# Kernel optimization log

Hardware: AMD Instinct MI355X
Metric: run time of the kernel (lower is better)

The kernel has to match this reference:

```python
import jax, jax.numpy as jnp
import numpy as np
import math

D_MODEL = 1024
N_HEADS = 16
D_KV = 64
NUM_BUCKETS = 32
MAX_DISTANCE = 128
BATCH = 4
SEQ = 2048


def _relative_position_bucket(relative_position, num_buckets=NUM_BUCKETS, max_distance=MAX_DISTANCE):
    # bidirectional=True (encoder)
    num_buckets //= 2
    relative_buckets = (relative_position > 0).astype(jnp.int32) * num_buckets
    rp = jnp.abs(relative_position)
    max_exact = num_buckets // 2
    is_small = rp < max_exact
    rp_safe = jnp.maximum(rp, 1)  # avoid log(0); masked by is_small anyway
    rp_if_large = max_exact + (
        jnp.log(rp_safe.astype(jnp.float32) / max_exact)
        / math.log(max_distance / max_exact)
        * (num_buckets - max_exact)
    ).astype(jnp.int32)
    rp_if_large = jnp.minimum(rp_if_large, num_buckets - 1)
    relative_buckets += jnp.where(is_small, rp, rp_if_large)
    return relative_buckets


def compute_bias(rel_bias, q_len, k_len):
    context = jnp.arange(q_len)[:, None]
    memory = jnp.arange(k_len)[None, :]
    buckets = _relative_position_bucket(memory - context)  # [q, k]
    values = rel_bias[buckets]                              # [q, k, h]
    return jnp.transpose(values, (2, 0, 1))[None]           # [1, h, q, k]


def setup_inputs() -> dict:
    key = jax.random.key(0)
    ks = jax.random.split(key, 6)
    s = 1.0 / math.sqrt(D_MODEL)
    return {
        "hidden_states": jax.random.normal(ks[0], (BATCH, SEQ, D_MODEL), jnp.float32),
        "wq": jax.random.normal(ks[1], (D_MODEL, N_HEADS * D_KV), jnp.float32) * s,
        "wk": jax.random.normal(ks[2], (D_MODEL, N_HEADS * D_KV), jnp.float32) * s,
        "wv": jax.random.normal(ks[3], (D_MODEL, N_HEADS * D_KV), jnp.float32) * s,
        "wo": jax.random.normal(ks[4], (N_HEADS * D_KV, D_MODEL), jnp.float32) * s,
        "rel_bias": jax.random.normal(ks[5], (NUM_BUCKETS, N_HEADS), jnp.float32) * 0.5,
    }


def reference(hidden_states, wq, wk, wv, wo, rel_bias):
    B, S, _ = hidden_states.shape

    def shape(x):  # [B,S,H*Dk] -> [B,H,S,Dk]
        return x.reshape(B, S, N_HEADS, D_KV).transpose(0, 2, 1, 3)

    q = shape(hidden_states @ wq)
    k = shape(hidden_states @ wk)
    v = shape(hidden_states @ wv)

    # NOTE: T5 does NOT scale by 1/sqrt(d_kv)
    scores = jnp.einsum("bhqd,bhkd->bhqk", q, k)
    position_bias = compute_bias(rel_bias, S, S)  # [1,H,S,S]
    scores = scores + position_bias
    attn = jax.nn.softmax(scores.astype(jnp.float32), axis=-1).astype(scores.dtype)
    ctx = jnp.einsum("bhqk,bhkd->bhqd", attn, v)
    ctx = ctx.transpose(0, 2, 1, 3).reshape(B, S, N_HEADS * D_KV)
    return ctx @ wo
```

## Files before the change

kernel.cpp:

```cpp
#include <hip/hip_runtime.h>
#include <hip/hip_bf16.h>

typedef unsigned short u16;
typedef unsigned int   u32;
typedef __bf16 bf16x8 __attribute__((ext_vector_type(8)));
typedef float  f32x4  __attribute__((ext_vector_type(4)));
typedef u16    u16x8  __attribute__((ext_vector_type(8)));
typedef u16    u16x4  __attribute__((ext_vector_type(4)));

#define MFMA16(a,b,c) __builtin_amdgcn_mfma_f32_16x16x32_bf16(a,b,c,0,0,0)
#define LOG2E 1.4426950408889634f

__device__ __forceinline__ u16 f2b(float f) {
    u32 u = __builtin_bit_cast(u32, f);
    u32 r = (u + 0x7FFFu + ((u >> 16) & 1u)) >> 16;
    return (u16)r;
}

typedef const __attribute__((address_space(1))) u32* gaddr_t;
typedef __attribute__((address_space(3))) u32*       laddr_t;
__device__ __forceinline__ void gl_lds16(const void* g, void* l) {
    __builtin_amdgcn_global_load_lds((gaddr_t)g, (laddr_t)l, 16, 0, 0);
}

__global__ __launch_bounds__(256) void prep_kernel(
        const float* __restrict__ H, const float* __restrict__ wq,
        const float* __restrict__ wk, const float* __restrict__ wv,
        const float* __restrict__ wo, const float* __restrict__ rel_bias,
        u16* __restrict__ Hb, u16* __restrict__ Wt, u16* __restrict__ Wot,
        float* __restrict__ tab) {
    __shared__ u16 tile[64 * 72];
    int bi = blockIdx.x;
    int t = threadIdx.x;
    if (bi < 4096) {
        int i = (bi * 256 + t) * 8;
        float4 a = *(const float4*)(H + i);
        float4 b = *(const float4*)(H + i + 4);
        u16x8 o = { f2b(a.x), f2b(a.y), f2b(a.z), f2b(a.w),
                    f2b(b.x), f2b(b.y), f2b(b.z), f2b(b.w) };
        *(u16x8*)(Hb + i) = o;
    } else if (bi < 5120) {
        int g2 = bi - 4096;
        int g = g2 >> 8, rem = g2 & 255;
        int n0 = (rem >> 4) * 64, k0 = (rem & 15) * 64;
        const float* src = (g == 0) ? wq : (g == 1) ? wk : (g == 2) ? wv : wo;
        u16* dst = (g < 3) ? (Wt + g * 1048576) : Wot;
#pragma unroll
        for (int rr = 0; rr < 4; ++rr) {
            int idx = rr * 256 + t;
            int kr = idx >> 4, c = idx & 15;
            float4 v = *(const float4*)(src + (k0 + kr) * 1024 + n0 + c * 4);
            u16x4 o = { f2b(v.x), f2b(v.y), f2b(v.z), f2b(v.w) };
            *(u16x4*)&tile[kr * 72 + c * 4] = o;
        }
        __syncthreads();
#pragma unroll
        for (int rr = 0; rr < 2; ++rr) {
            int idx = rr * 256 + t;
            int n = idx >> 3, c = idx & 7;
            u16x8 o;
#pragma unroll
            for (int j = 0; j < 8; ++j) o[j] = tile[(c * 8 + j) * 72 + n];
            *(u16x8*)(dst + (n0 + n) * 1024 + k0 + c * 8) = o;
        }
    } else {
        int i = (bi - 5120) * 256 + t;
        int h = i >> 12;
        int idx = i & 4095;
        int delta = idx - 2048;
        int bucket = (delta > 0) ? 16 : 0;
        int rp = delta < 0 ? -delta : delta;
        if (rp < 8) {
            bucket += rp;
        } else {
            double v = log((double)rp / 8.0) / log(16.0) * 8.0;
            int tt = (int)v;
            int b2 = 8 + tt;
            bucket += (b2 < 15) ? b2 : 15;
        }
        tab[h * 4096 + idx] = rel_bias[bucket * 16 + h] * LOG2E;
    }
}

template <int MODE>
__global__ __launch_bounds__(256) void gemm_bt(
        const u16* __restrict__ A, const u16* __restrict__ Bt, int K, int N,
        u16* __restrict__ q_out, u16* __restrict__ k_out, u16* __restrict__ v_out,
        float* __restrict__ f_out) {
    __shared__ u16 As[128 * 32];
    __shared__ u16 Bs[128 * 32];
    __shared__ u16 vt_tile[MODE == 0 ? 128 * 136 : 1];
    int t = threadIdx.x;
    int lane = t & 63, w = t >> 6;
    int wm = w & 1, wn = w >> 1;
    int ln = lane & 15, quad = lane >> 4;
    int m0 = blockIdx.x * 128, n0 = blockIdx.y * 128;
    const u16* Ab = A + m0 * K;
    const u16* Bb = Bt + n0 * K;
    f32x4 acc[4][4] = {};
    int nk = K >> 5;
    for (int kt = 0; kt < nk; ++kt) {
        int k0 = kt * 32;
#pragma unroll
        for (int rr = 0; rr < 2; ++rr) {
            int idx = rr * 256 + t;
            int row = idx >> 2, c = (idx & 3) ^ (row & 3);
            gl_lds16(Ab + row * K + k0 + c * 8, ((char*)As) + idx * 16);
            gl_lds16(Bb + row * K + k0 + c * 8, ((char*)Bs) + idx * 16);
        }
        __syncthreads();
        bf16x8 af[4], bfr[4];
#pragma unroll
        for (int mb = 0; mb < 4; ++mb) {
            int row = wm * 64 + mb * 16 + ln;
            af[mb] = *(const bf16x8*)&As[row * 32 + ((quad ^ (row & 3)) << 3)];
        }
#pragma unroll
        for (int nb = 0; nb < 4; ++nb) {
            int row = wn * 64 + nb * 16 + ln;
            bfr[nb] = *(const bf16x8*)&Bs[row * 32 + ((quad ^ (row & 3)) << 3)];
        }
#pragma unroll
        for (int mb = 0; mb < 4; ++mb)
#pragma unroll
            for (int nb = 0; nb < 4; ++nb)
                acc[mb][nb] = MFMA16(af[mb], bfr[nb], acc[mb][nb]);
        __syncthreads();
    }
    if (MODE == 0 && n0 >= 2048) {
#pragma unroll
        for (int mb = 0; mb < 4; ++mb)
#pragma unroll
            for (int nb = 0; nb < 4; ++nb)
#pragma unroll
                for (int r = 0; r < 4; ++r) {
                    int np = wn * 64 + nb * 16 + ln;
                    int mp = wm * 64 + mb * 16 + quad * 4 + r;
                    vt_tile[np * 136 + mp] = f2b(acc[mb][nb][r]);
                }
        __syncthreads();
        int h0 = (n0 >> 6) & 15;
        int b = m0 >> 11;
        int s0 = m0 & 2047;
#pragma unroll
        for (int j = 0; j < 8; ++j) {
            int e = j * 256 + t;
            int d_all = e >> 4;
            int sc = e & 15;
            int hh = h0 + (d_all >> 6);
            int d = d_all & 63;
            u16x8 val = *(const u16x8*)&vt_tile[d_all * 136 + sc * 8];
            *(u16x8*)(v_out + (b * 16 + hh) * 131072 + d * 2048 + s0 + sc * 8) = val;
        }
    } else {
#pragma unroll
        for (int mb = 0; mb < 4; ++mb)
#pragma unroll
            for (int nb = 0; nb < 4; ++nb)
#pragma unroll
                for (int r = 0; r < 4; ++r) {
                    int m = m0 + wm * 64 + mb * 16 + quad * 4 + r;
                    int n = n0 + wn * 64 + nb * 16 + ln;
                    float v = acc[mb][nb][r];
                    if (MODE == 0) {
                        int which = n >> 10, h = (n >> 6) & 15, d = n & 63;
                        int b = m >> 11, s = m & 2047;
                        u16* dst = (which == 0) ? q_out : k_out;
                        float scale = (which == 0) ? LOG2E : 1.0f;
                        dst[(((b << 4) + h) * 2048 + s) * 64 + d] = f2b(v * scale);
                    } else {
                        f_out[m * N + n] = v;
                    }
                }
    }
}

__global__ __launch_bounds__(256, 3) void attn_kernel(
        const u16* __restrict__ Qb, const u16* __restrict__ Kb,
        const u16* __restrict__ Vt, const float* __restrict__ bias_tab,
        u16* __restrict__ ctx) {
    __shared__ u16 Ks[128 * 64];
    __shared__ u16 Vs[64 * 128];
    __shared__ u16 Ps[4][16 * 64];
    __shared__ float sb[2176];
    int t = threadIdx.x;
    int lane = t & 63, w = t >> 6;
    int ln = lane & 15, quad = lane >> 4;
    int bh = blockIdx.x >> 5;
    int qtile = blockIdx.x & 31;
    int h = bh & 15, b = bh >> 4;
    int q0 = qtile * 64;

    float chi = bias_tab[h * 4096 + 2048 + 1500];
    float clo = bias_tab[h * 4096 + 2048 - 1500];

    const float* tb = bias_tab + h * 4096 + (1985 - q0);
    for (int i = t; i < 2175; i += 256) sb[i] = tb[i];

    int qa = q0 + w * 16 + ln;
    const u16* qptr = Qb + (bh * 2048 + qa) * 64 + quad * 8;
    bf16x8 qf0 = *(const bf16x8*)(qptr);
    bf16x8 qf1 = *(const bf16x8*)(qptr + 32);

    const u16* Kbase = Kb + bh * 2048 * 64;
    const u16* Vbase = Vt + bh * 64 * 2048;

    f32x4 oacc[4] = {};
    float l_i = 0.0f;
    int cb_base = 63 - w * 16 + quad * 4 - ln;
    int swl = ln & 7;

    for (int kt = 0; kt < 16; ++kt) {
        int kb0 = kt * 128;
#pragma unroll
        for (int it = 0; it < 4; ++it) {
            int idx = it * 256 + t;
            int row = idx >> 3, c = (idx & 7) ^ (row & 7);
            gl_lds16(Kbase + (kb0 + row) * 64 + c * 8, ((char*)Ks) + idx * 16);
        }
#pragma unroll
        for (int it = 0; it < 4; ++it) {
            int idx = it * 256 + t;
            int row = idx >> 4, c = (idx & 15) ^ (row & 7);
            gl_lds16(Vbase + row * 2048 + kb0 + c * 8, ((char*)Vs) + idx * 16);
        }
        __syncthreads();

        f32x4 sacc[8];
        int diff = kb0 - q0;
        if (diff >= 192 || diff <= -256) {
            float c0 = (diff > 0) ? chi : clo;
            f32x4 ci = {c0, c0, c0, c0};
#pragma unroll
            for (int nb = 0; nb < 8; ++nb) {
                int key = nb * 16 + ln;
                int sw = key & 7;
                bf16x8 kf0 = *(const bf16x8*)&Ks[key * 64 + ((quad ^ sw) << 3)];
                bf16x8 kf1 = *(const bf16x8*)&Ks[key * 64 + (((quad ^ 4) ^ sw) << 3)];
                f32x4 scc = MFMA16(kf0, qf0, ci);
                sacc[nb] = MFMA16(kf1, qf1, scc);
            }
        } else {
            int cb = kb0 + cb_base;
#pragma unroll
            for (int nb = 0; nb < 8; ++nb) {
                int key = nb * 16 + ln;
                int sw = key & 7;
                const float* bp = &sb[cb + nb * 16];
                f32x4 ci = {bp[0], bp[1], bp[2], bp[3]};
                bf16x8 kf0 = *(const bf16x8*)&Ks[key * 64 + ((quad ^ sw) << 3)];
                bf16x8 kf1 = *(const bf16x8*)&Ks[key * 64 + (((quad ^ 4) ^ sw) << 3)];
                f32x4 scc = MFMA16(kf0, qf0, ci);
                sacc[nb] = MFMA16(kf1, qf1, scc);
            }
        }

        float p[8][4];
        float ls0 = 0.f, ls1 = 0.f, ls2 = 0.f, ls3 = 0.f;
#pragma unroll
        for (int nb = 0; nb < 8; ++nb) {
            float e0 = __builtin_amdgcn_exp2f(sacc[nb][0]);
            float e1 = __builtin_amdgcn_exp2f(sacc[nb][1]);
            float e2 = __builtin_amdgcn_exp2f(sacc[nb][2]);
            float e3 = __builtin_amdgcn_exp2f(sacc[nb][3]);
            p[nb][0] = e0; p[nb][1] = e1; p[nb][2] = e2; p[nb][3] = e3;
            ls0 += e0; ls1 += e1; ls2 += e2; ls3 += e3;
        }
        l_i += (ls0 + ls1) + (ls2 + ls3);

        u16* pw = &Ps[w][0];
#pragma unroll
        for (int half = 0; half < 2; ++half) {
#pragma unroll
            for (int nbh = 0; nbh < 4; ++nbh) {
                int nb = half * 4 + nbh;
                u32 a0 = __builtin_bit_cast(u32, p[nb][0]) + 0x8000u;
                u32 a1 = __builtin_bit_cast(u32, p[nb][1]) + 0x8000u;
                u32 a2 = __builtin_bit_cast(u32, p[nb][2]) + 0x8000u;
                u32 a3 = __builtin_bit_cast(u32, p[nb][3]) + 0x8000u;
                u32 lo = __builtin_amdgcn_perm(a1, a0, 0x07060302);
                u32 hi = __builtin_amdgcn_perm(a3, a2, 0x07060302);
                int c = nbh * 2 + (quad >> 1);
                u32* dst = (u32*)&pw[ln * 64 + ((c ^ swl) << 3) + (quad & 1) * 4];
                dst[0] = lo;
                dst[1] = hi;
            }
#pragma unroll
            for (int kc = 0; kc < 2; ++kc) {
                bf16x8 pf = *(const bf16x8*)&pw[ln * 64 + (((kc * 4 + quad) ^ swl) << 3)];
#pragma unroll
                for (int nb = 0; nb < 4; ++nb) {
                    int d = nb * 16 + ln;
                    int vc = (half * 8 + kc * 4 + quad) ^ (d & 7);
                    bf16x8 vf = *(const bf16x8*)&Vs[d * 128 + (vc << 3)];
                    oacc[nb] = MFMA16(pf, vf, oacc[nb]);
                }
            }
        }
        __syncthreads();
    }

    l_i += __shfl_xor(l_i, 16);
    l_i += __shfl_xor(l_i, 32);
    float linv = 1.0f / l_i;
#pragma unroll
    for (int r = 0; r < 4; ++r) {
        float lr = __shfl(linv, quad * 4 + r);
        int q = q0 + w * 16 + quad * 4 + r;
#pragma unroll
        for (int nb = 0; nb < 4; ++nb)
            ctx[(b * 2048 + q) * 1024 + h * 64 + nb * 16 + ln] = f2b(oacc[nb][r] * lr);
    }
}

extern "C" void kernel_launch(void* const* d_in, const int* in_sizes, int n_in,
                              void* d_out, int out_size, void* d_ws, size_t ws_size,
                              hipStream_t stream) {
    const float* H   = (const float*)d_in[0];
    const float* wq  = (const float*)d_in[1];
    const float* wk  = (const float*)d_in[2];
    const float* wv  = (const float*)d_in[3];
    const float* wo  = (const float*)d_in[4];
    const float* rel = (const float*)d_in[5];
    float* out = (float*)d_out;

    char* ws = (char*)d_ws;
    u16* Hb    = (u16*)(ws);
    u16* Wt    = (u16*)(ws + 16777216);
    u16* Wot   = (u16*)(ws + 23068672);
    u16* Qb    = (u16*)(ws + 25165824);
    u16* Kb    = (u16*)(ws + 41943040);
    u16* Vt    = (u16*)(ws + 58720256);
    float* bias_tab = (float*)(ws + 75497472);
    u16* ctx = Hb;

    prep_kernel<<<5376, 256, 0, stream>>>(H, wq, wk, wv, wo, rel, Hb, Wt, Wot, bias_tab);
    gemm_bt<0><<<dim3(64, 24), 256, 0, stream>>>(Hb, Wt, 1024, 3072, Qb, Kb, Vt, nullptr);
    attn_kernel<<<2048, 256, 0, stream>>>(Qb, Kb, Vt, bias_tab, ctx);
    gemm_bt<1><<<dim3(64, 8), 256, 0, stream>>>(ctx, Wot, 1024, 1024, nullptr, nullptr, nullptr, out);
}
```

Baseline: 303.2 us.

## Process two 64-row query tiles per attention block to reuse K/V LDS loads

Each attention block now handles 128 queries (two 64-row sub-tiles A and B) instead of 64, so each K/V tile staged in shared memory is reused for twice as many queries. The grid is halved accordingly and the bias table window is shifted to cover both sub-tiles. The aim is to cut global-to-LDS traffic and barrier count per query. In exchange, register pressure roughly doubles for accumulators and Q fragments, which may reduce occupancy under launch bounds of 3 blocks per CU, and the grid of 1024 blocks gives fewer waves to balance across CUs.

```diff
diff --git a/kernel.cpp b/kernel.cpp
--- a/kernel.cpp
+++ b/kernel.cpp
@@ -186,27 +186,30 @@
     int t = threadIdx.x;
     int lane = t & 63, w = t >> 6;
     int ln = lane & 15, quad = lane >> 4;
-    int bh = blockIdx.x >> 5;
-    int qtile = blockIdx.x & 31;
+    int bh = blockIdx.x >> 4;
+    int qt = blockIdx.x & 15;
     int h = bh & 15, b = bh >> 4;
-    int q0 = qtile * 64;
+    int Q0 = qt * 128;
 
     float chi = bias_tab[h * 4096 + 2048 + 1500];
     float clo = bias_tab[h * 4096 + 2048 - 1500];
 
-    const float* tb = bias_tab + h * 4096 + (1985 - q0);
+    const float* tb = bias_tab + h * 4096 + (1921 - Q0);
     for (int i = t; i < 2175; i += 256) sb[i] = tb[i];
 
-    int qa = q0 + w * 16 + ln;
-    const u16* qptr = Qb + (bh * 2048 + qa) * 64 + quad * 8;
-    bf16x8 qf0 = *(const bf16x8*)(qptr);
-    bf16x8 qf1 = *(const bf16x8*)(qptr + 32);
+    const u16* qpA = Qb + (bh * 2048 + Q0 + w * 16 + ln) * 64 + quad * 8;
+    bf16x8 qfA0 = *(const bf16x8*)(qpA);
+    bf16x8 qfA1 = *(const bf16x8*)(qpA + 32);
+    const u16* qpB = qpA + 4096;
+    bf16x8 qfB0 = *(const bf16x8*)(qpB);
+    bf16x8 qfB1 = *(const bf16x8*)(qpB + 32);
 
     const u16* Kbase = Kb + bh * 2048 * 64;
     const u16* Vbase = Vt + bh * 64 * 2048;
 
-    f32x4 oacc[4] = {};
-    float l_i = 0.0f;
+    f32x4 oaccA[4] = {};
+    f32x4 oaccB[4] = {};
+    float lA = 0.0f, lB = 0.0f;
     int cb_base = 63 - w * 16 + quad * 4 - ln;
     int swl = ln & 7;
 
@@ -226,90 +229,179 @@
         }
         __syncthreads();
 
-        f32x4 sacc[8];
-        int diff = kb0 - q0;
-        if (diff >= 192 || diff <= -256) {
-            float c0 = (diff > 0) ? chi : clo;
-            f32x4 ci = {c0, c0, c0, c0};
+        {
+            f32x4 sacc[8];
+            int diff = kb0 - Q0;
+            if (diff >= 192 || diff <= -256) {
+                float c0 = (diff > 0) ? chi : clo;
+                f32x4 ci = {c0, c0, c0, c0};
+#pragma unroll
+                for (int nb = 0; nb < 8; ++nb) {
+                    int key = nb * 16 + ln;
+                    int sw = key & 7;
+                    bf16x8 kf0 = *(const bf16x8*)&Ks[key * 64 + ((quad ^ sw) << 3)];
+                    bf16x8 kf1 = *(const bf16x8*)&Ks[key * 64 + (((quad ^ 4) ^ sw) << 3)];
+                    f32x4 scc = MFMA16(kf0, qfA0, ci);
+                    sacc[nb] = MFMA16(kf1, qfA1, scc);
+                }
+            } else {
+                int cb = kb0 + cb_base + 64;
+#pragma unroll
+                for (int nb = 0; nb < 8; ++nb) {
+                    int key = nb * 16 + ln;
+                    int sw = key & 7;
+                    const float* bp = &sb[cb + nb * 16];
+                    f32x4 ci = {bp[0], bp[1], bp[2], bp[3]};
+                    bf16x8 kf0 = *(const bf16x8*)&Ks[key * 64 + ((quad ^ sw) << 3)];
+                    bf16x8 kf1 = *(const bf16x8*)&Ks[key * 64 + (((quad ^ 4) ^ sw) << 3)];
+                    f32x4 scc = MFMA16(kf0, qfA0, ci);
+                    sacc[nb] = MFMA16(kf1, qfA1, scc);
+                }
+            }
+            float p[8][4];
+            float ls0 = 0.f, ls1 = 0.f, ls2 = 0.f, ls3 = 0.f;
 #pragma unroll
             for (int nb = 0; nb < 8; ++nb) {
-                int key = nb * 16 + ln;
-                int sw = key & 7;
-                bf16x8 kf0 = *(const bf16x8*)&Ks[key * 64 + ((quad ^ sw) << 3)];
-                bf16x8 kf1 = *(const bf16x8*)&Ks[key * 64 + (((quad ^ 4) ^ sw) << 3)];
-                f32x4 scc = MFMA16(kf0, qf0, ci);
-                sacc[nb] = MFMA16(kf1, qf1, scc);
-            }
-        } else {
-            int cb = kb0 + cb_base;
+                float e0 = __builtin_amdgcn_exp2f(sacc[nb][0]);
+                float e1 = __builtin_amdgcn_exp2f(sacc[nb][1]);
+                float e2 = __builtin_amdgcn_exp2f(sacc[nb][2]);
+                float e3 = __builtin_amdgcn_exp2f(sacc[nb][3]);
+                p[nb][0] = e0; p[nb][1] = e1; p[nb][2] = e2; p[nb][3] = e3;
+                ls0 += e0; ls1 += e1; ls2 += e2; ls3 += e3;
+            }
+            lA += (ls0 + ls1) + (ls2 + ls3);
+            u16* pw = &Ps[w][0];
+#pragma unroll
+            for (int half = 0; half < 2; ++half) {
+#pragma unroll
+                for (int nbh = 0; nbh < 4; ++nbh) {
+                    int nb = half * 4 + nbh;
+                    u32 a0 = __builtin_bit_cast(u32, p[nb][0]) + 0x8000u;
+                    u32 a1 = __builtin_bit_cast(u32, p[nb][1]) + 0x8000u;
+                    u32 a2 = __builtin_bit_cast(u32, p[nb][2]) + 0x8000u;
+                    u32 a3 = __builtin_bit_cast(u32, p[nb][3]) + 0x8000u;
+                    u32 lo = __builtin_amdgcn_perm(a1, a0, 0x07060302);
+                    u32 hi = __builtin_amdgcn_perm(a3, a2, 0x07060302);
+                    int c = nbh * 2 + (quad >> 1);
+                    u32* dst = (u32*)&pw[ln * 64 + ((c ^ swl) << 3) + (quad & 1) * 4];
+                    dst[0] = lo;
+                    dst[1] = hi;
+                }
+#pragma unroll
+                for (int kc = 0; kc < 2; ++kc) {
+                    bf16x8 pf = *(const bf16x8*)&pw[ln * 64 + (((kc * 4 + quad) ^ swl) << 3)];
+#pragma unroll
+                    for (int nb = 0; nb < 4; ++nb) {
+                        int d = nb * 16 + ln;
+                        int vc = (half * 8 + kc * 4 + quad) ^ (d & 7);
+                        bf16x8 vf = *(const bf16x8*)&Vs[d * 128 + (vc << 3)];
+                        oaccA[nb] = MFMA16(pf, vf, oaccA[nb]);
+                    }
+                }
+            }
+        }
+
+        {
+            f32x4 sacc[8];
+            int diff = kb0 - Q0 - 64;
+            if (diff >= 192 || diff <= -256) {
+                float c0 = (diff > 0) ? chi : clo;
+                f32x4 ci = {c0, c0, c0, c0};
+#pragma unroll
+                for (int nb = 0; nb < 8; ++nb) {
+                    int key = nb * 16 + ln;
+                    int sw = key & 7;
+                    bf16x8 kf0 = *(const bf16x8*)&Ks[key * 64 + ((quad ^ sw) << 3)];
+                    bf16x8 kf1 = *(const bf16x8*)&Ks[key * 64 + (((quad ^ 4) ^ sw) << 3)];
+                    f32x4 scc = MFMA16(kf0, qfB0, ci);
+                    sacc[nb] = MFMA16(kf1, qfB1, scc);
+                }
+            } else {
+                int cb = kb0 + cb_base;
+#pragma unroll
+                for (int nb = 0; nb < 8; ++nb) {
+                    int key = nb * 16 + ln;
+                    int sw = key & 7;
+                    const float* bp = &sb[cb + nb * 16];
+                    f32x4 ci = {bp[0], bp[1], bp[2], bp[3]};
+                    bf16x8 kf0 = *(const bf16x8*)&Ks[key * 64 + ((quad ^ sw) << 3)];
+                    bf16x8 kf1 = *(const bf16x8*)&Ks[key * 64 + (((quad ^ 4) ^ sw) << 3)];
+                    f32x4 scc = MFMA16(kf0, qfB0, ci);
+                    sacc[nb] = MFMA16(kf1, qfB1, scc);
+                }
+            }
+            float p[8][4];
+            float ls0 = 0.f, ls1 = 0.f, ls2 = 0.f, ls3 = 0.f;
 #pragma unroll
             for (int nb = 0; nb < 8; ++nb) {
-                int key = nb * 16 + ln;
-                int sw = key & 7;
-                const float* bp = &sb[cb + nb * 16];
-                f32x4 ci = {bp[0], bp[1], bp[2], bp[3]};
-                bf16x8 kf0 = *(const bf16x8*)&Ks[key * 64 + ((quad ^ sw) << 3)];
-                bf16x8 kf1 = *(const bf16x8*)&Ks[key * 64 + (((quad ^ 4) ^ sw) << 3)];
-                f32x4 scc = MFMA16(kf0, qf0, ci);
-                sacc[nb] = MFMA16(kf1, qf1, scc);
-            }
-        }
-
-        float p[8][4];
-        float ls0 = 0.f, ls1 = 0.f, ls2 = 0.f, ls3 = 0.f;
-#pragma unroll
-        for (int nb = 0; nb < 8; ++nb) {
-            float e0 = __builtin_amdgcn_exp2f(sacc[nb][0]);
-            float e1 = __builtin_amdgcn_exp2f(sacc[nb][1]);
-            float e2 = __builtin_amdgcn_exp2f(sacc[nb][2]);
-            float e3 = __builtin_amdgcn_exp2f(sacc[nb][3]);
-            p[nb][0] = e0; p[nb][1] = e1; p[nb][2] = e2; p[nb][3] = e3;
-            ls0 += e0; ls1 += e1; ls2 += e2; ls3 += e3;
-        }
-        l_i += (ls0 + ls1) + (ls2 + ls3);
-
-        u16* pw = &Ps[w][0];
-#pragma unroll
-        for (int half = 0; half < 2; ++half) {
-#pragma unroll
-            for (int nbh = 0; nbh < 4; ++nbh) {
-                int nb = half * 4 + nbh;
-                u32 a0 = __builtin_bit_cast(u32, p[nb][0]) + 0x8000u;
-                u32 a1 = __builtin_bit_cast(u32, p[nb][1]) + 0x8000u;
-                u32 a2 = __builtin_bit_cast(u32, p[nb][2]) + 0x8000u;
-                u32 a3 = __builtin_bit_cast(u32, p[nb][3]) + 0x8000u;
-                u32 lo = __builtin_amdgcn_perm(a1, a0, 0x07060302);
-                u32 hi = __builtin_amdgcn_perm(a3, a2, 0x07060302);
-                int c = nbh * 2 + (quad >> 1);
-                u32* dst = (u32*)&pw[ln * 64 + ((c ^ swl) << 3) + (quad & 1) * 4];
-                dst[0] = lo;
-                dst[1] = hi;
-            }
-#pragma unroll
-            for (int kc = 0; kc < 2; ++kc) {
-                bf16x8 pf = *(const bf16x8*)&pw[ln * 64 + (((kc * 4 + quad) ^ swl) << 3)];
-#pragma unroll
-                for (int nb = 0; nb < 4; ++nb) {
-                    int d = nb * 16 + ln;
-                    int vc = (half * 8 + kc * 4 + quad) ^ (d & 7);
-                    bf16x8 vf = *(const bf16x8*)&Vs[d * 128 + (vc << 3)];
-                    oacc[nb] = MFMA16(pf, vf, oacc[nb]);
-                }
-            }
-        }
-        __syncthreads();
-    }
-
-    l_i += __shfl_xor(l_i, 16);
-    l_i += __shfl_xor(l_i, 32);
-    float linv = 1.0f / l_i;
-#pragma unroll
-    for (int r = 0; r < 4; ++r) {
-        float lr = __shfl(linv, quad * 4 + r);
-        int q = q0 + w * 16 + quad * 4 + r;
-#pragma unroll
-        for (int nb = 0; nb < 4; ++nb)
-            ctx[(b * 2048 + q) * 1024 + h * 64 + nb * 16 + ln] = f2b(oacc[nb][r] * lr);
+                float e0 = __builtin_amdgcn_exp2f(sacc[nb][0]);
+                float e1 = __builtin_amdgcn_exp2f(sacc[nb][1]);
+                float e2 = __builtin_amdgcn_exp2f(sacc[nb][2]);
+                float e3 = __builtin_amdgcn_exp2f(sacc[nb][3]);
+                p[nb][0] = e0; p[nb][1] = e1; p[nb][2] = e2; p[nb][3] = e3;
+                ls0 += e0; ls1 += e1; ls2 += e2; ls3 += e3;
+            }
+            lB += (ls0 + ls1) + (ls2 + ls3);
+            u16* pw = &Ps[w][0];
+#pragma unroll
+            for (int half = 0; half < 2; ++half) {
+#pragma unroll
+                for (int nbh = 0; nbh < 4; ++nbh) {
+                    int nb = half * 4 + nbh;
+                    u32 a0 = __builtin_bit_cast(u32, p[nb][0]) + 0x8000u;
+                    u32 a1 = __builtin_bit_cast(u32, p[nb][1]) + 0x8000u;
+                    u32 a2 = __builtin_bit_cast(u32, p[nb][2]) + 0x8000u;
+                    u32 a3 = __builtin_bit_cast(u32, p[nb][3]) + 0x8000u;
+                    u32 lo = __builtin_amdgcn_perm(a1, a0, 0x07060302);
+                    u32 hi = __builtin_amdgcn_perm(a3, a2, 0x07060302);
+                    int c = nbh * 2 + (quad >> 1);
+                    u32* dst = (u32*)&pw[ln * 64 + ((c ^ swl) << 3) + (quad & 1) * 4];
+                    dst[0] = lo;
+                    dst[1] = hi;
+                }
+#pragma unroll
+                for (int kc = 0; kc < 2; ++kc) {
+                    bf16x8 pf = *(const bf16x8*)&pw[ln * 64 + (((kc * 4 + quad) ^ swl) << 3)];
+#pragma unroll
+                    for (int nb = 0; nb < 4; ++nb) {
+                        int d = nb * 16 + ln;
+                        int vc = (half * 8 + kc * 4 + quad) ^ (d & 7);
+                        bf16x8 vf = *(const bf16x8*)&Vs[d * 128 + (vc << 3)];
+                        oaccB[nb] = MFMA16(pf, vf, oaccB[nb]);
+                    }
+                }
+            }
+        }
+        __syncthreads();
+    }
+
+    {
+        float l = lA;
+        l += __shfl_xor(l, 16);
+        l += __shfl_xor(l, 32);
+        float linv = 1.0f / l;
+#pragma unroll
+        for (int r = 0; r < 4; ++r) {
+            float lr = __shfl(linv, quad * 4 + r);
+            int q = Q0 + w * 16 + quad * 4 + r;
+#pragma unroll
+            for (int nb = 0; nb < 4; ++nb)
+                ctx[(b * 2048 + q) * 1024 + h * 64 + nb * 16 + ln] = f2b(oaccA[nb][r] * lr);
+        }
+    }
+    {
+        float l = lB;
+        l += __shfl_xor(l, 16);
+        l += __shfl_xor(l, 32);
+        float linv = 1.0f / l;
+#pragma unroll
+        for (int r = 0; r < 4; ++r) {
+            float lr = __shfl(linv, quad * 4 + r);
+            int q = Q0 + 64 + w * 16 + quad * 4 + r;
+#pragma unroll
+            for (int nb = 0; nb < 4; ++nb)
+                ctx[(b * 2048 + q) * 1024 + h * 64 + nb * 16 + ln] = f2b(oaccB[nb][r] * lr);
+        }
     }
 }
 
@@ -336,6 +428,6 @@
 
     prep_kernel<<<5376, 256, 0, stream>>>(H, wq, wk, wv, wo, rel, Hb, Wt, Wot, bias_tab);
     gemm_bt<0><<<dim3(64, 24), 256, 0, stream>>>(Hb, Wt, 1024, 3072, Qb, Kb, Vt, nullptr);
-    attn_kernel<<<2048, 256, 0, stream>>>(Qb, Kb, Vt, bias_tab, ctx);
+    attn_kernel<<<1024, 256, 0, stream>>>(Qb, Kb, Vt, bias_tab, ctx);
     gemm_bt<1><<<dim3(64, 8), 256, 0, stream>>>(ctx, Wot, 1024, 1024, nullptr, nullptr, nullptr, out);
 }
```

Result: no change. 305.8 us (+0.9%).
